# Performance work log

Measured on AMD Instinct MI355X. Metric: run time of the kernel, lower is better.

## Reference

```python
import jax, jax.numpy as jnp
import numpy as np

B, H, W, N, C = 2, 56, 56, 2, 128
NUM_HEADS = 8
SPLIT = 7
IDX = 0  # 0 -> H_sp = H, W_sp = split_size (vertical stripes)


def setup_inputs() -> dict:
    key = jax.random.key(0)
    k1, k2, k3, k4 = jax.random.split(key, 4)
    query = jax.random.normal(k1, (B, H, W, N, C), jnp.float32)
    key_t = jax.random.normal(k2, (B, H, W, N, C), jnp.float32)
    value = jax.random.normal(k3, (B, H, W, N, C), jnp.float32)
    conv_w = jax.random.normal(k4, (C, 1, 3, 3), jnp.float32) * 0.1  # depthwise get_v weight
    return {"query": query, "key": key_t, "value": value, "conv_w": conv_w}


def _im2cswin(x, Hsp, Wsp, h):
    # [b, Hp, Wp, n, c] -> [(b i j), h, Hsp*Wsp*n, d]
    b, Hp, Wp, n, c = x.shape
    i, j = Hp // Hsp, Wp // Wsp
    d = c // h
    x = x.reshape(b, i, Hsp, j, Wsp, n, h, d)
    x = x.transpose(0, 1, 3, 6, 2, 4, 5, 7)  # b i j h Hsp Wsp n d
    return x.reshape(b * i * j, h, Hsp * Wsp * n, d)


def _window_mask(Hsp, Wsp, n):
    # block attention between same spatial position / different candidates (except diagonal)
    pos = jnp.repeat(jnp.arange(Hsp * Wsp), n)
    L = pos.shape[0]
    m = jnp.where(pos[:, None] == pos[None, :], -jnp.inf, 0.0).astype(jnp.float32)
    m = m.at[jnp.arange(L), jnp.arange(L)].set(0.0)
    return m


def reference(query, key, value, conv_w):
    b, Hh, Ww, n, c = query.shape
    if IDX == -1:
        Hsp, Wsp = Hh, Ww
    elif IDX == 0:
        Hsp, Wsp = Hh, SPLIT
    else:
        Hsp, Wsp = SPLIT, Ww
    # H % Hsp == 0 and W % Wsp == 0 by construction -> no padding branch
    h = NUM_HEADS
    d = c // h
    scale = d ** (-0.5)

    q = _im2cswin(query, Hsp, Wsp, h)
    k = _im2cswin(key, Hsp, Wsp, h)
    v = _im2cswin(value, Hsp, Wsp, h)

    # rpe via depthwise 3x3 conv over the value (LePE-style), summed over candidates
    v_img = value.transpose(0, 3, 4, 1, 2).reshape(b * n, c, Hh, Ww)  # [b*n, C, H, W]
    conv = jax.lax.conv_general_dilated(
        v_img, conv_w, (1, 1), 'SAME',
        dimension_numbers=('NCHW', 'OIHW', 'NCHW'), feature_group_count=c)
    rpe = conv.reshape(b, n, c, Hh, Ww).sum(1, keepdims=True)
    center = conv_w[:, 0, 1, 1]  # center tap of each depthwise kernel
    self_scaled = (v_img * center[None, :, None, None]).reshape(b, n, c, Hh, Ww)
    self_scaled = self_scaled - self_scaled.sum(1, keepdims=True)
    rpe = (rpe + self_scaled).transpose(0, 3, 4, 1, 2)  # [b, H, W, n, c]

    mask = _window_mask(Hsp, Wsp, n)[None, None]  # [1,1,L,L]
    attn = jnp.einsum('bhid,bhjd->bhij', q * scale, k) + mask
    attn = jax.nn.softmax(attn.astype(jnp.float32), axis=-1).astype(q.dtype)
    x = jnp.einsum('bhij,bhjd->bhid', attn, v)

    # windows back to image layout
    i, j = Hh // Hsp, Ww // Wsp
    x = x.reshape(b, i, j, h, Hsp, Wsp, n, d)
    x = x.transpose(0, 1, 4, 2, 5, 6, 3, 7).reshape(b, Hh, Ww, n, c)
    return x + rpe
```

## Files before the change

kernel.cpp:

```cpp
#include <hip/hip_runtime.h>

typedef __bf16 bf16x8 __attribute__((ext_vector_type(8)));
typedef float f32x16 __attribute__((ext_vector_type(16)));
typedef unsigned u32x2 __attribute__((ext_vector_type(2)));

#define BB 2
#define HH 56
#define WW 56
#define NN 2
#define CC 128
#define NH 8
#define DD 16
#define WSP 7
#define LQ 784
#define KB_TOK 800
#define VT_STRIDE 808
#define NKC 25
#define NINST 128
#define BPI 5
#define NWAVE 5

#define K_OFF 0
#define V_OFF 25600
#define W_OFF 51456
#define ONES_OFF 52032
#define SMEM_BYTES 52064

#define QSCALE 0.3606737602222409f

union U2 { __bf16 h[2]; unsigned u; };
union U4 { unsigned u[4]; bf16x8 v; };
union H8 { bf16x8 v; uint4 q; };

static __device__ __forceinline__ float4 f4zero() { float4 r; r.x = r.y = r.z = r.w = 0.f; return r; }
static __device__ __forceinline__ float4 f4add(float4 a, float4 b) {
    float4 r; r.x = a.x + b.x; r.y = a.y + b.y; r.z = a.z + b.z; r.w = a.w + b.w; return r;
}
static __device__ __forceinline__ float4 f4fma(float4 acc, float4 w, float4 s) {
    acc.x += w.x * s.x; acc.y += w.y * s.y; acc.z += w.z * s.z; acc.w += w.w * s.w; return acc;
}

__global__ __launch_bounds__(320) void attn_fused(const float* __restrict__ q_g,
                                                  const float* __restrict__ k_g,
                                                  const float* __restrict__ v_g,
                                                  const float* __restrict__ conv_w,
                                                  float* __restrict__ out) {
    __shared__ alignas(16) char smem[SMEM_BYTES];
    __bf16* Klds = (__bf16*)(smem + K_OFF);
    __bf16* Vlds = (__bf16*)(smem + V_OFF);
    float*  wlds = (float*)(smem + W_OFF);
    __bf16* onesb = (__bf16*)(smem + ONES_OFF);

    const int bid  = blockIdx.x;
    const int g    = bid >> 3;
    const int inst = (bid & 7) + 8 * (g / BPI);
    const int part = g % BPI;
    const int head = inst & 7;
    const int win  = inst >> 3;
    const int b    = win >> 3, wj = win & 7;
    const int tid  = threadIdx.x;

    if (tid < 144) {
        int c = tid & 15, k = tid >> 4;
        wlds[k * 16 + c] = conv_w[(head * 16 + c) * 9 + k];
    } else if (tid < 160) {
        onesb[tid - 144] = (__bf16)1.f;
    }

    for (int tok = tid; tok < KB_TOK; tok += 320) {
        if (tok < LQ) {
            int pos = tok >> 1, n = tok & 1;
            int y = pos / WSP, xl2 = pos - y * WSP;
            long off = ((long)(((b * HH + y) * WW + wj * WSP + xl2) * NN + n)) * CC + head * DD;

            float kv[16], vv[16];
            *(float4*)&kv[0]  = *(const float4*)(k_g + off);
            *(float4*)&kv[4]  = *(const float4*)(k_g + off + 4);
            *(float4*)&kv[8]  = *(const float4*)(k_g + off + 8);
            *(float4*)&kv[12] = *(const float4*)(k_g + off + 12);
            *(float4*)&vv[0]  = *(const float4*)(v_g + off);
            *(float4*)&vv[4]  = *(const float4*)(v_g + off + 4);
            *(float4*)&vv[8]  = *(const float4*)(v_g + off + 8);
            *(float4*)&vv[12] = *(const float4*)(v_g + off + 12);

            H8 lo, hi;
#pragma unroll
            for (int i = 0; i < 8; ++i) { lo.v[i] = (__bf16)kv[i]; hi.v[i] = (__bf16)kv[8 + i]; }
            *(uint4*)&Klds[tok * 16]     = lo.q;
            *(uint4*)&Klds[tok * 16 + 8] = hi.q;
#pragma unroll
            for (int d = 0; d < 16; ++d)
                Vlds[d * VT_STRIDE + tok] = (__bf16)vv[d];
        } else {
            H8 z; z.q = make_uint4(0, 0, 0, 0);
            *(uint4*)&Klds[tok * 16]     = z.q;
            *(uint4*)&Klds[tok * 16 + 8] = z.q;
#pragma unroll
            for (int d = 0; d < 16; ++d)
                Vlds[d * VT_STRIDE + tok] = (__bf16)0.f;
        }
    }
    __syncthreads();

    const int w    = tid >> 6;
    const int lane = tid & 63;
    const int col  = lane & 31;
    const int h    = lane >> 5;
    const int qt   = part * NWAVE + w;
    const int myq  = qt * 32 + col;
    const int sib  = myq ^ 1;

    const int myqc = myq < LQ ? myq : LQ - 1;
    const int pos = myqc >> 1, n = myqc & 1;
    const int y = pos / WSP, xl = pos - y * WSP;
    const long ooff = ((long)(((b * HH + y) * WW + wj * WSP + xl) * NN + n)) * CC + head * DD;

    bf16x8 qfv;
    {
        const float* qp = q_g + ooff + 8 * h;
        float qv[8];
        *(float4*)&qv[0] = *(const float4*)qp;
        *(float4*)&qv[4] = *(const float4*)(qp + 4);
        H8 qq;
#pragma unroll
        for (int i = 0; i < 8; ++i) qq.v[i] = (__bf16)(qv[i] * QSCALE);
        qfv = qq.v;
    }

    f32x16 acc, zv;
#pragma unroll
    for (int i = 0; i < 16; ++i) { acc[i] = 0.f; zv[i] = 0.f; }

    const char* kbase = (const char*)Klds + col * 32 + h * 16;
    const char* vbase;
    int vstep, tstep;
    if (col < 16) {
        vbase = (const char*)Vlds + col * (VT_STRIDE * 2) + h * 16;
        vstep = 64; tstep = 32;
    } else {
        vbase = (const char*)onesb;
        vstep = 0; tstep = 0;
    }

    for (int c = 0; c < NKC; ++c) {
        bf16x8 kf = *(const bf16x8*)(kbase + c * 1024);

        f32x16 st = __builtin_amdgcn_mfma_f32_32x32x16_bf16(kf, qfv, zv, 0, 0, 0);

        float p[16];
        if (c == qt || c == NKC - 1) {
#pragma unroll
            for (int r = 0; r < 16; ++r) {
                int kr = (r & 3) + 8 * (r >> 2) + 4 * h;
                int gk = c * 32 + kr;
                p[r] = (gk >= LQ || gk == sib) ? 0.f : __builtin_amdgcn_exp2f(st[r]);
            }
        } else {
#pragma unroll
            for (int r = 0; r < 16; ++r) p[r] = __builtin_amdgcn_exp2f(st[r]);
        }

        unsigned pk[4][2];
#pragma unroll
        for (int b2 = 0; b2 < 4; ++b2) {
            U2 a, bb;
            a.h[0]  = (__bf16)p[4 * b2 + 0];
            a.h[1]  = (__bf16)p[4 * b2 + 1];
            bb.h[0] = (__bf16)p[4 * b2 + 2];
            bb.h[1] = (__bf16)p[4 * b2 + 3];
            pk[b2][0] = a.u;
            pk[b2][1] = bb.u;
        }

#pragma unroll
        for (int t = 0; t < 2; ++t) {
            U4 pb;
#pragma unroll
            for (int j = 0; j < 2; ++j) {
#if __has_builtin(__builtin_amdgcn_permlane32_swap)
                u32x2 rr = __builtin_amdgcn_permlane32_swap(pk[2 * t][j], pk[2 * t + 1][j], false, false);
                pb.u[j]     = rr[0];
                pb.u[2 + j] = rr[1];
#else
                unsigned swa = __shfl_xor(pk[2 * t][j], 32, 64);
                unsigned swb = __shfl_xor(pk[2 * t + 1][j], 32, 64);
                pb.u[j]     = h ? swb : pk[2 * t][j];
                pb.u[2 + j] = h ? pk[2 * t + 1][j] : swa;
#endif
            }
            bf16x8 vf = *(const bf16x8*)(vbase + c * vstep + t * tstep);
            acc = __builtin_amdgcn_mfma_f32_32x32x16_bf16(vf, pb.v, acc, 0, 0, 0);
        }
    }

    if (myq < LQ) {
        const int xg = wj * WSP + xl;
        const long rowbase = ((long)(b * HH + y) * WW + xg) * (NN * CC) + head * DD;

        float4 cv0 = f4zero(), cv1 = f4zero();
        float4 sc0 = f4zero(), sc1 = f4zero();
        float4 vn0 = f4zero(), vn1 = f4zero();

#pragma unroll
        for (int dy = -1; dy <= 1; ++dy) {
            int yy = y + dy;
#pragma unroll
            for (int dx = -1; dx <= 1; ++dx) {
                int xx = xg + dx;
                if (yy < 0 || yy >= HH || xx < 0 || xx >= WW) continue;
                int k = (dy + 1) * 3 + (dx + 1);
                const float* p = v_g + rowbase + ((long)dy * WW + dx) * (NN * CC);
                float4 a0 = *(const float4*)(p + 4 * h);
                float4 b0 = *(const float4*)(p + CC + 4 * h);
                float4 a1 = *(const float4*)(p + 8 + 4 * h);
                float4 b1 = *(const float4*)(p + CC + 8 + 4 * h);
                float4 w0 = *(const float4*)(wlds + k * 16 + 4 * h);
                float4 w1 = *(const float4*)(wlds + k * 16 + 8 + 4 * h);
                float4 S0 = f4add(a0, b0);
                float4 S1 = f4add(a1, b1);
                cv0 = f4fma(cv0, w0, S0);
                cv1 = f4fma(cv1, w1, S1);
                if (dy == 0 && dx == 0) {
                    sc0 = S0; sc1 = S1;
                    vn0 = n ? b0 : a0;
                    vn1 = n ? b1 : a1;
                }
            }
        }
        float4 wc0 = *(const float4*)(wlds + 4 * 16 + 4 * h);
        float4 wc1 = *(const float4*)(wlds + 4 * 16 + 8 + 4 * h);

        float inv = 1.f / acc[8];
        float* po = out + ooff;
        float4 r0, r1;
        r0.x = cv0.x + wc0.x * (vn0.x - sc0.x) + acc[0] * inv;
        r0.y = cv0.y + wc0.y * (vn0.y - sc0.y) + acc[1] * inv;
        r0.z = cv0.z + wc0.z * (vn0.z - sc0.z) + acc[2] * inv;
        r0.w = cv0.w + wc0.w * (vn0.w - sc0.w) + acc[3] * inv;
        r1.x = cv1.x + wc1.x * (vn1.x - sc1.x) + acc[4] * inv;
        r1.y = cv1.y + wc1.y * (vn1.y - sc1.y) + acc[5] * inv;
        r1.z = cv1.z + wc1.z * (vn1.z - sc1.z) + acc[6] * inv;
        r1.w = cv1.w + wc1.w * (vn1.w - sc1.w) + acc[7] * inv;
        *(float4*)(po + 4 * h) = r0;
        *(float4*)(po + 8 + 4 * h) = r1;
    }
}

extern "C" void kernel_launch(void* const* d_in, const int* in_sizes, int n_in,
                              void* d_out, int out_size, void* d_ws, size_t ws_size,
                              hipStream_t stream) {
    const float* q = (const float*)d_in[0];
    const float* k = (const float*)d_in[1];
    const float* v = (const float*)d_in[2];
    const float* w = (const float*)d_in[3];
    float* out = (float*)d_out;

    attn_fused<<<NINST * BPI, 320, 0, stream>>>(q, k, v, w, out);
}
```

Measured before the change: 37.71 us.

## Hoist depthwise conv before attention loop and split MFMA accumulator in two

Moves the LePE depthwise 3x3 conv gather from the epilogue to before the K/V staging loop. It uses branch-free clamped addresses with a zero multiplier, so its global loads overlap the LDS fill and the main loop instead of sitting serially at the end. The attention chunk loop is also unrolled into two independent accumulators, summed at the end, to break the MFMA accumulation dependency chain. In exchange, conv results stay live across the main loop, adding register pressure, and the loads at image borders are always issued.

```diff
diff --git a/kernel.cpp b/kernel.cpp
--- a/kernel.cpp
+++ b/kernel.cpp
@@ -36,8 +36,8 @@
 static __device__ __forceinline__ float4 f4add(float4 a, float4 b) {
     float4 r; r.x = a.x + b.x; r.y = a.y + b.y; r.z = a.z + b.z; r.w = a.w + b.w; return r;
 }
-static __device__ __forceinline__ float4 f4fma(float4 acc, float4 w, float4 s) {
-    acc.x += w.x * s.x; acc.y += w.y * s.y; acc.z += w.z * s.z; acc.w += w.w * s.w; return acc;
+static __device__ __forceinline__ float4 f4fmas(float4 acc, float4 w, float s, float4 S) {
+    acc.x += w.x * s * S.x; acc.y += w.y * s * S.y; acc.z += w.z * s * S.z; acc.w += w.w * s * S.w; return acc;
 }
 
 __global__ __launch_bounds__(320) void attn_fused(const float* __restrict__ q_g,
@@ -66,12 +66,57 @@
     } else if (tid < 160) {
         onesb[tid - 144] = (__bf16)1.f;
     }
+    __syncthreads();
+
+    const int w    = tid >> 6;
+    const int lane = tid & 63;
+    const int col  = lane & 31;
+    const int h    = lane >> 5;
+    const int qt   = part * NWAVE + w;
+    const int myq  = qt * 32 + col;
+    const int sib  = myq ^ 1;
+
+    const int myqc = myq < LQ ? myq : LQ - 1;
+    const int pos = myqc >> 1, n = myqc & 1;
+    const int y = pos / WSP, xl = pos - y * WSP;
+    const long ooff = ((long)(((b * HH + y) * WW + wj * WSP + xl) * NN + n)) * CC + head * DD;
+
+    float4 cv0 = f4zero(), cv1 = f4zero();
+    float4 sc0, sc1, vn0, vn1;
+    {
+        const int xg = wj * WSP + xl;
+        const long rowbase = ((long)(b * HH + y) * WW + xg) * (NN * CC) + head * DD;
+#pragma unroll
+        for (int k = 0; k < 9; ++k) {
+            int dy = k / 3 - 1, dx = k % 3 - 1;
+            int yy = y + dy, xx = xg + dx;
+            bool ok = (yy >= 0 && yy < HH && xx >= 0 && xx < WW);
+            int yc = ok ? yy : y, xc = ok ? xx : xg;
+            float m = ok ? 1.f : 0.f;
+            const float* p = v_g + rowbase + ((long)(yc - y) * WW + (xc - xg)) * (NN * CC);
+            float4 a0 = *(const float4*)(p + 4 * h);
+            float4 b0 = *(const float4*)(p + CC + 4 * h);
+            float4 a1 = *(const float4*)(p + 8 + 4 * h);
+            float4 b1 = *(const float4*)(p + CC + 8 + 4 * h);
+            float4 w0 = *(const float4*)(wlds + k * 16 + 4 * h);
+            float4 w1 = *(const float4*)(wlds + k * 16 + 8 + 4 * h);
+            float4 S0 = f4add(a0, b0);
+            float4 S1 = f4add(a1, b1);
+            cv0 = f4fmas(cv0, w0, m, S0);
+            cv1 = f4fmas(cv1, w1, m, S1);
+            if (k == 4) {
+                sc0 = S0; sc1 = S1;
+                vn0 = n ? b0 : a0;
+                vn1 = n ? b1 : a1;
+            }
+        }
+    }
 
     for (int tok = tid; tok < KB_TOK; tok += 320) {
         if (tok < LQ) {
-            int pos = tok >> 1, n = tok & 1;
-            int y = pos / WSP, xl2 = pos - y * WSP;
-            long off = ((long)(((b * HH + y) * WW + wj * WSP + xl2) * NN + n)) * CC + head * DD;
+            int tpos = tok >> 1, tn = tok & 1;
+            int ty = tpos / WSP, txl = tpos - ty * WSP;
+            long off = ((long)(((b * HH + ty) * WW + wj * WSP + txl) * NN + tn)) * CC + head * DD;
 
             float kv[16], vv[16];
             *(float4*)&kv[0]  = *(const float4*)(k_g + off);
@@ -102,19 +147,6 @@
     }
     __syncthreads();
 
-    const int w    = tid >> 6;
-    const int lane = tid & 63;
-    const int col  = lane & 31;
-    const int h    = lane >> 5;
-    const int qt   = part * NWAVE + w;
-    const int myq  = qt * 32 + col;
-    const int sib  = myq ^ 1;
-
-    const int myqc = myq < LQ ? myq : LQ - 1;
-    const int pos = myqc >> 1, n = myqc & 1;
-    const int y = pos / WSP, xl = pos - y * WSP;
-    const long ooff = ((long)(((b * HH + y) * WW + wj * WSP + xl) * NN + n)) * CC + head * DD;
-
     bf16x8 qfv;
     {
         const float* qp = q_g + ooff + 8 * h;
@@ -127,9 +159,9 @@
         qfv = qq.v;
     }
 
-    f32x16 acc, zv;
-#pragma unroll
-    for (int i = 0; i < 16; ++i) { acc[i] = 0.f; zv[i] = 0.f; }
+    f32x16 acc0, acc1, zv;
+#pragma unroll
+    for (int i = 0; i < 16; ++i) { acc0[i] = 0.f; acc1[i] = 0.f; zv[i] = 0.f; }
 
     const char* kbase = (const char*)Klds + col * 32 + h * 16;
     const char* vbase;
@@ -142,9 +174,8 @@
         vstep = 0; tstep = 0;
     }
 
-    for (int c = 0; c < NKC; ++c) {
+    auto do_chunk = [&](int c, f32x16& acc) {
         bf16x8 kf = *(const bf16x8*)(kbase + c * 1024);
-
         f32x16 st = __builtin_amdgcn_mfma_f32_32x32x16_bf16(kf, qfv, zv, 0, 0, 0);
 
         float p[16];
@@ -191,56 +222,29 @@
             bf16x8 vf = *(const bf16x8*)(vbase + c * vstep + t * tstep);
             acc = __builtin_amdgcn_mfma_f32_32x32x16_bf16(vf, pb.v, acc, 0, 0, 0);
         }
-    }
+    };
+
+    for (int it = 0; it < 12; ++it) {
+        do_chunk(2 * it, acc0);
+        do_chunk(2 * it + 1, acc1);
+    }
+    do_chunk(24, acc0);
 
     if (myq < LQ) {
-        const int xg = wj * WSP + xl;
-        const long rowbase = ((long)(b * HH + y) * WW + xg) * (NN * CC) + head * DD;
-
-        float4 cv0 = f4zero(), cv1 = f4zero();
-        float4 sc0 = f4zero(), sc1 = f4zero();
-        float4 vn0 = f4zero(), vn1 = f4zero();
-
-#pragma unroll
-        for (int dy = -1; dy <= 1; ++dy) {
-            int yy = y + dy;
-#pragma unroll
-            for (int dx = -1; dx <= 1; ++dx) {
-                int xx = xg + dx;
-                if (yy < 0 || yy >= HH || xx < 0 || xx >= WW) continue;
-                int k = (dy + 1) * 3 + (dx + 1);
-                const float* p = v_g + rowbase + ((long)dy * WW + dx) * (NN * CC);
-                float4 a0 = *(const float4*)(p + 4 * h);
-                float4 b0 = *(const float4*)(p + CC + 4 * h);
-                float4 a1 = *(const float4*)(p + 8 + 4 * h);
-                float4 b1 = *(const float4*)(p + CC + 8 + 4 * h);
-                float4 w0 = *(const float4*)(wlds + k * 16 + 4 * h);
-                float4 w1 = *(const float4*)(wlds + k * 16 + 8 + 4 * h);
-                float4 S0 = f4add(a0, b0);
-                float4 S1 = f4add(a1, b1);
-                cv0 = f4fma(cv0, w0, S0);
-                cv1 = f4fma(cv1, w1, S1);
-                if (dy == 0 && dx == 0) {
-                    sc0 = S0; sc1 = S1;
-                    vn0 = n ? b0 : a0;
-                    vn1 = n ? b1 : a1;
-                }
-            }
-        }
+        float lsum = acc0[8] + acc1[8];
+        float inv = 1.f / lsum;
         float4 wc0 = *(const float4*)(wlds + 4 * 16 + 4 * h);
         float4 wc1 = *(const float4*)(wlds + 4 * 16 + 8 + 4 * h);
-
-        float inv = 1.f / acc[8];
         float* po = out + ooff;
         float4 r0, r1;
-        r0.x = cv0.x + wc0.x * (vn0.x - sc0.x) + acc[0] * inv;
-        r0.y = cv0.y + wc0.y * (vn0.y - sc0.y) + acc[1] * inv;
-        r0.z = cv0.z + wc0.z * (vn0.z - sc0.z) + acc[2] * inv;
-        r0.w = cv0.w + wc0.w * (vn0.w - sc0.w) + acc[3] * inv;
-        r1.x = cv1.x + wc1.x * (vn1.x - sc1.x) + acc[4] * inv;
-        r1.y = cv1.y + wc1.y * (vn1.y - sc1.y) + acc[5] * inv;
-        r1.z = cv1.z + wc1.z * (vn1.z - sc1.z) + acc[6] * inv;
-        r1.w = cv1.w + wc1.w * (vn1.w - sc1.w) + acc[7] * inv;
+        r0.x = cv0.x + wc0.x * (vn0.x - sc0.x) + (acc0[0] + acc1[0]) * inv;
+        r0.y = cv0.y + wc0.y * (vn0.y - sc0.y) + (acc0[1] + acc1[1]) * inv;
+        r0.z = cv0.z + wc0.z * (vn0.z - sc0.z) + (acc0[2] + acc1[2]) * inv;
+        r0.w = cv0.w + wc0.w * (vn0.w - sc0.w) + (acc0[3] + acc1[3]) * inv;
+        r1.x = cv1.x + wc1.x * (vn1.x - sc1.x) + (acc0[4] + acc1[4]) * inv;
+        r1.y = cv1.y + wc1.y * (vn1.y - sc1.y) + (acc0[5] + acc1[5]) * inv;
+        r1.z = cv1.z + wc1.z * (vn1.z - sc1.z) + (acc0[6] + acc1[6]) * inv;
+        r1.w = cv1.w + wc1.w * (vn1.w - sc1.w) + (acc0[7] + acc1[7]) * inv;
         *(float4*)(po + 4 * h) = r0;
         *(float4*)(po + 8 + 4 * h) = r1;
     }
```

Measured after the change: 61.28 us. +62.5%, slower.

## Split key loop across two waves per query tile and load K directly from global

Applied to the files above, without the earlier changes.

Doubles the block to 640 threads so each 32-query tile is handled by two waves that process alternating key chunks, then combines their partial accumulators through shared memory before the epilogue. K is no longer staged in LDS; each wave loads and converts its key fragment straight from global memory inside the loop, which shrinks LDS usage. The intent is more parallelism and shorter per-wave serial loops. In exchange it adds an extra barrier and reduction step, and puts scattered global K loads on the critical path of the MFMA loop.

```diff
diff --git a/kernel.cpp b/kernel.cpp
--- a/kernel.cpp
+++ b/kernel.cpp
@@ -18,13 +18,13 @@
 #define NKC 25
 #define NINST 128
 #define BPI 5
-#define NWAVE 5
-
-#define K_OFF 0
-#define V_OFF 25600
-#define W_OFF 51456
-#define ONES_OFF 52032
-#define SMEM_BYTES 52064
+#define NTHR 640
+
+#define V_OFF 0
+#define W_OFF 25856
+#define ONES_OFF 26432
+#define RED_OFF 26464
+#define SMEM_BYTES 39264
 
 #define QSCALE 0.3606737602222409f
 
@@ -40,16 +40,16 @@
     acc.x += w.x * s.x; acc.y += w.y * s.y; acc.z += w.z * s.z; acc.w += w.w * s.w; return acc;
 }
 
-__global__ __launch_bounds__(320) void attn_fused(const float* __restrict__ q_g,
-                                                  const float* __restrict__ k_g,
-                                                  const float* __restrict__ v_g,
-                                                  const float* __restrict__ conv_w,
-                                                  float* __restrict__ out) {
+__global__ __launch_bounds__(NTHR) void attn_fused(const float* __restrict__ q_g,
+                                                   const float* __restrict__ k_g,
+                                                   const float* __restrict__ v_g,
+                                                   const float* __restrict__ conv_w,
+                                                   float* __restrict__ out) {
     __shared__ alignas(16) char smem[SMEM_BYTES];
-    __bf16* Klds = (__bf16*)(smem + K_OFF);
-    __bf16* Vlds = (__bf16*)(smem + V_OFF);
-    float*  wlds = (float*)(smem + W_OFF);
+    __bf16* Vlds  = (__bf16*)(smem + V_OFF);
+    float*  wlds  = (float*)(smem + W_OFF);
     __bf16* onesb = (__bf16*)(smem + ONES_OFF);
+    float*  red   = (float*)(smem + RED_OFF);
 
     const int bid  = blockIdx.x;
     const int g    = bid >> 3;
@@ -67,34 +67,20 @@
         onesb[tid - 144] = (__bf16)1.f;
     }
 
-    for (int tok = tid; tok < KB_TOK; tok += 320) {
+    for (int tok = tid; tok < KB_TOK; tok += NTHR) {
         if (tok < LQ) {
-            int pos = tok >> 1, n = tok & 1;
-            int y = pos / WSP, xl2 = pos - y * WSP;
-            long off = ((long)(((b * HH + y) * WW + wj * WSP + xl2) * NN + n)) * CC + head * DD;
-
-            float kv[16], vv[16];
-            *(float4*)&kv[0]  = *(const float4*)(k_g + off);
-            *(float4*)&kv[4]  = *(const float4*)(k_g + off + 4);
-            *(float4*)&kv[8]  = *(const float4*)(k_g + off + 8);
-            *(float4*)&kv[12] = *(const float4*)(k_g + off + 12);
+            int tpos = tok >> 1, tn = tok & 1;
+            int ty = tpos / WSP, txl = tpos - ty * WSP;
+            long off = ((long)(((b * HH + ty) * WW + wj * WSP + txl) * NN + tn)) * CC + head * DD;
+            float vv[16];
             *(float4*)&vv[0]  = *(const float4*)(v_g + off);
             *(float4*)&vv[4]  = *(const float4*)(v_g + off + 4);
             *(float4*)&vv[8]  = *(const float4*)(v_g + off + 8);
             *(float4*)&vv[12] = *(const float4*)(v_g + off + 12);
-
-            H8 lo, hi;
-#pragma unroll
-            for (int i = 0; i < 8; ++i) { lo.v[i] = (__bf16)kv[i]; hi.v[i] = (__bf16)kv[8 + i]; }
-            *(uint4*)&Klds[tok * 16]     = lo.q;
-            *(uint4*)&Klds[tok * 16 + 8] = hi.q;
 #pragma unroll
             for (int d = 0; d < 16; ++d)
                 Vlds[d * VT_STRIDE + tok] = (__bf16)vv[d];
         } else {
-            H8 z; z.q = make_uint4(0, 0, 0, 0);
-            *(uint4*)&Klds[tok * 16]     = z.q;
-            *(uint4*)&Klds[tok * 16 + 8] = z.q;
 #pragma unroll
             for (int d = 0; d < 16; ++d)
                 Vlds[d * VT_STRIDE + tok] = (__bf16)0.f;
@@ -102,13 +88,15 @@
     }
     __syncthreads();
 
-    const int w    = tid >> 6;
-    const int lane = tid & 63;
-    const int col  = lane & 31;
-    const int h    = lane >> 5;
-    const int qt   = part * NWAVE + w;
-    const int myq  = qt * 32 + col;
-    const int sib  = myq ^ 1;
+    const int w     = tid >> 6;
+    const int lane  = tid & 63;
+    const int col   = lane & 31;
+    const int h     = lane >> 5;
+    const int tile  = w >> 1;
+    const int khalf = w & 1;
+    const int qt    = part * BPI + tile;
+    const int myq   = qt * 32 + col;
+    const int sib   = myq ^ 1;
 
     const int myqc = myq < LQ ? myq : LQ - 1;
     const int pos = myqc >> 1, n = myqc & 1;
@@ -131,7 +119,6 @@
 #pragma unroll
     for (int i = 0; i < 16; ++i) { acc[i] = 0.f; zv[i] = 0.f; }
 
-    const char* kbase = (const char*)Klds + col * 32 + h * 16;
     const char* vbase;
     int vstep, tstep;
     if (col < 16) {
@@ -142,8 +129,22 @@
         vstep = 0; tstep = 0;
     }
 
-    for (int c = 0; c < NKC; ++c) {
-        bf16x8 kf = *(const bf16x8*)(kbase + c * 1024);
+    for (int c = khalf; c < NKC; c += 2) {
+        bf16x8 kf;
+        {
+            int tok = c * 32 + col;
+            int tokc = tok < LQ ? tok : LQ - 1;
+            int tpos = tokc >> 1, tn = tokc & 1;
+            int ty = tpos / WSP, txl = tpos - ty * WSP;
+            long koff = ((long)(((b * HH + ty) * WW + wj * WSP + txl) * NN + tn)) * CC + head * DD + 8 * h;
+            float kv[8];
+            *(float4*)&kv[0] = *(const float4*)(k_g + koff);
+            *(float4*)&kv[4] = *(const float4*)(k_g + koff + 4);
+            H8 kk;
+#pragma unroll
+            for (int i = 0; i < 8; ++i) kk.v[i] = (__bf16)kv[i];
+            kf = kk.v;
+        }
 
         f32x16 st = __builtin_amdgcn_mfma_f32_32x32x16_bf16(kf, qfv, zv, 0, 0, 0);
 
@@ -193,7 +194,20 @@
         }
     }
 
-    if (myq < LQ) {
+    if (khalf) {
+        float* rp = red + (tile * 64 + lane) * 10;
+#pragma unroll
+        for (int i = 0; i < 9; ++i) rp[i] = acc[i];
+    }
+    __syncthreads();
+
+    if (!khalf && myq < LQ) {
+        const float* rp = red + (tile * 64 + lane) * 10;
+        float o[9];
+#pragma unroll
+        for (int i = 0; i < 9; ++i) o[i] = acc[i] + rp[i];
+        float inv = 1.f / o[8];
+
         const int xg = wj * WSP + xl;
         const long rowbase = ((long)(b * HH + y) * WW + xg) * (NN * CC) + head * DD;
 
@@ -230,17 +244,16 @@
         float4 wc0 = *(const float4*)(wlds + 4 * 16 + 4 * h);
         float4 wc1 = *(const float4*)(wlds + 4 * 16 + 8 + 4 * h);
 
-        float inv = 1.f / acc[8];
         float* po = out + ooff;
         float4 r0, r1;
-        r0.x = cv0.x + wc0.x * (vn0.x - sc0.x) + acc[0] * inv;
-        r0.y = cv0.y + wc0.y * (vn0.y - sc0.y) + acc[1] * inv;
-        r0.z = cv0.z + wc0.z * (vn0.z - sc0.z) + acc[2] * inv;
-        r0.w = cv0.w + wc0.w * (vn0.w - sc0.w) + acc[3] * inv;
-        r1.x = cv1.x + wc1.x * (vn1.x - sc1.x) + acc[4] * inv;
-        r1.y = cv1.y + wc1.y * (vn1.y - sc1.y) + acc[5] * inv;
-        r1.z = cv1.z + wc1.z * (vn1.z - sc1.z) + acc[6] * inv;
-        r1.w = cv1.w + wc1.w * (vn1.w - sc1.w) + acc[7] * inv;
+        r0.x = cv0.x + wc0.x * (vn0.x - sc0.x) + o[0] * inv;
+        r0.y = cv0.y + wc0.y * (vn0.y - sc0.y) + o[1] * inv;
+        r0.z = cv0.z + wc0.z * (vn0.z - sc0.z) + o[2] * inv;
+        r0.w = cv0.w + wc0.w * (vn0.w - sc0.w) + o[3] * inv;
+        r1.x = cv1.x + wc1.x * (vn1.x - sc1.x) + o[4] * inv;
+        r1.y = cv1.y + wc1.y * (vn1.y - sc1.y) + o[5] * inv;
+        r1.z = cv1.z + wc1.z * (vn1.z - sc1.z) + o[6] * inv;
+        r1.w = cv1.w + wc1.w * (vn1.w - sc1.w) + o[7] * inv;
         *(float4*)(po + 4 * h) = r0;
         *(float4*)(po + 8 + 4 * h) = r1;
     }
@@ -255,5 +268,5 @@
     const float* w = (const float*)d_in[3];
     float* out = (float*)d_out;
 
-    attn_fused<<<NINST * BPI, 320, 0, stream>>>(q, k, v, w, out);
-}
+    attn_fused<<<NINST * BPI, NTHR, 0, stream>>>(q, k, v, w, out);
+}
```

Measured after the change: 45.51 us. 1.21x slower.

## Pre-pack K to bf16 in workspace and read K fragments directly from global

Applied to the files above, without the earlier changes.

Adds a separate pack_k kernel that converts K to bf16 in per-window/head token order in the workspace. The attention kernel no longer stages K in LDS; each wave reads its MFMA K fragments straight from the packed global buffer, which halves LDS use and may allow more resident blocks. The cost is an extra launch plus a global round-trip for K. The fragment loads now sit inside the main loop and rely on cache hits, since five blocks share each instance's K.

```diff
diff --git a/kernel.cpp b/kernel.cpp
--- a/kernel.cpp
+++ b/kernel.cpp
@@ -19,12 +19,12 @@
 #define NINST 128
 #define BPI 5
 #define NWAVE 5
-
-#define K_OFF 0
-#define V_OFF 25600
-#define W_OFF 51456
-#define ONES_OFF 52032
-#define SMEM_BYTES 52064
+#define KW_UNITS 1600
+
+#define V_OFF 0
+#define W_OFF 25856
+#define ONES_OFF 26432
+#define SMEM_BYTES 26464
 
 #define QSCALE 0.3606737602222409f
 
@@ -40,15 +40,45 @@
     acc.x += w.x * s.x; acc.y += w.y * s.y; acc.z += w.z * s.z; acc.w += w.w * s.w; return acc;
 }
 
+__global__ __launch_bounds__(256) void pack_k(const float* __restrict__ k_g,
+                                              uint4* __restrict__ kws) {
+    int idx = blockIdx.x * blockDim.x + threadIdx.x;
+    if (idx >= NINST * KB_TOK) return;
+    int inst = idx / KB_TOK;
+    int tok  = idx - inst * KB_TOK;
+    uint4* dst = kws + (long)inst * KW_UNITS + tok * 2;
+
+    if (tok >= LQ) {
+        uint4 z = make_uint4(0, 0, 0, 0);
+        dst[0] = z; dst[1] = z;
+        return;
+    }
+    int head = inst & 7, win = inst >> 3;
+    int b = win >> 3, wj = win & 7;
+    int pos = tok >> 1, n = tok & 1;
+    int y = pos / WSP, xl = pos - y * WSP;
+    long off = ((long)(((b * HH + y) * WW + wj * WSP + xl) * NN + n)) * CC + head * DD;
+
+    float kv[16];
+    *(float4*)&kv[0]  = *(const float4*)(k_g + off);
+    *(float4*)&kv[4]  = *(const float4*)(k_g + off + 4);
+    *(float4*)&kv[8]  = *(const float4*)(k_g + off + 8);
+    *(float4*)&kv[12] = *(const float4*)(k_g + off + 12);
+    H8 lo, hi;
+#pragma unroll
+    for (int i = 0; i < 8; ++i) { lo.v[i] = (__bf16)kv[i]; hi.v[i] = (__bf16)kv[8 + i]; }
+    dst[0] = lo.q;
+    dst[1] = hi.q;
+}
+
 __global__ __launch_bounds__(320) void attn_fused(const float* __restrict__ q_g,
-                                                  const float* __restrict__ k_g,
+                                                  const uint4* __restrict__ kws,
                                                   const float* __restrict__ v_g,
                                                   const float* __restrict__ conv_w,
                                                   float* __restrict__ out) {
     __shared__ alignas(16) char smem[SMEM_BYTES];
-    __bf16* Klds = (__bf16*)(smem + K_OFF);
-    __bf16* Vlds = (__bf16*)(smem + V_OFF);
-    float*  wlds = (float*)(smem + W_OFF);
+    __bf16* Vlds  = (__bf16*)(smem + V_OFF);
+    float*  wlds  = (float*)(smem + W_OFF);
     __bf16* onesb = (__bf16*)(smem + ONES_OFF);
 
     const int bid  = blockIdx.x;
@@ -69,32 +99,18 @@
 
     for (int tok = tid; tok < KB_TOK; tok += 320) {
         if (tok < LQ) {
-            int pos = tok >> 1, n = tok & 1;
-            int y = pos / WSP, xl2 = pos - y * WSP;
-            long off = ((long)(((b * HH + y) * WW + wj * WSP + xl2) * NN + n)) * CC + head * DD;
-
-            float kv[16], vv[16];
-            *(float4*)&kv[0]  = *(const float4*)(k_g + off);
-            *(float4*)&kv[4]  = *(const float4*)(k_g + off + 4);
-            *(float4*)&kv[8]  = *(const float4*)(k_g + off + 8);
-            *(float4*)&kv[12] = *(const float4*)(k_g + off + 12);
+            int tpos = tok >> 1, tn = tok & 1;
+            int ty = tpos / WSP, txl = tpos - ty * WSP;
+            long off = ((long)(((b * HH + ty) * WW + wj * WSP + txl) * NN + tn)) * CC + head * DD;
+            float vv[16];
             *(float4*)&vv[0]  = *(const float4*)(v_g + off);
             *(float4*)&vv[4]  = *(const float4*)(v_g + off + 4);
             *(float4*)&vv[8]  = *(const float4*)(v_g + off + 8);
             *(float4*)&vv[12] = *(const float4*)(v_g + off + 12);
-
-            H8 lo, hi;
-#pragma unroll
-            for (int i = 0; i < 8; ++i) { lo.v[i] = (__bf16)kv[i]; hi.v[i] = (__bf16)kv[8 + i]; }
-            *(uint4*)&Klds[tok * 16]     = lo.q;
-            *(uint4*)&Klds[tok * 16 + 8] = hi.q;
 #pragma unroll
             for (int d = 0; d < 16; ++d)
                 Vlds[d * VT_STRIDE + tok] = (__bf16)vv[d];
         } else {
-            H8 z; z.q = make_uint4(0, 0, 0, 0);
-            *(uint4*)&Klds[tok * 16]     = z.q;
-            *(uint4*)&Klds[tok * 16 + 8] = z.q;
 #pragma unroll
             for (int d = 0; d < 16; ++d)
                 Vlds[d * VT_STRIDE + tok] = (__bf16)0.f;
@@ -131,7 +147,7 @@
 #pragma unroll
     for (int i = 0; i < 16; ++i) { acc[i] = 0.f; zv[i] = 0.f; }
 
-    const char* kbase = (const char*)Klds + col * 32 + h * 16;
+    const uint4* kbase = kws + (long)inst * KW_UNITS + (col * 2 + h);
     const char* vbase;
     int vstep, tstep;
     if (col < 16) {
@@ -143,9 +159,9 @@
     }
 
     for (int c = 0; c < NKC; ++c) {
-        bf16x8 kf = *(const bf16x8*)(kbase + c * 1024);
-
-        f32x16 st = __builtin_amdgcn_mfma_f32_32x32x16_bf16(kf, qfv, zv, 0, 0, 0);
+        U4 kf;
+        *(uint4*)&kf = kbase[c * 64];
+        f32x16 st = __builtin_amdgcn_mfma_f32_32x32x16_bf16(kf.v, qfv, zv, 0, 0, 0);
 
         float p[16];
         if (c == qt || c == NKC - 1) {
@@ -194,6 +210,8 @@
     }
 
     if (myq < LQ) {
+        float inv = 1.f / acc[8];
+
         const int xg = wj * WSP + xl;
         const long rowbase = ((long)(b * HH + y) * WW + xg) * (NN * CC) + head * DD;
 
@@ -230,7 +248,6 @@
         float4 wc0 = *(const float4*)(wlds + 4 * 16 + 4 * h);
         float4 wc1 = *(const float4*)(wlds + 4 * 16 + 8 + 4 * h);
 
-        float inv = 1.f / acc[8];
         float* po = out + ooff;
         float4 r0, r1;
         r0.x = cv0.x + wc0.x * (vn0.x - sc0.x) + acc[0] * inv;
@@ -254,6 +271,10 @@
     const float* v = (const float*)d_in[2];
     const float* w = (const float*)d_in[3];
     float* out = (float*)d_out;
-
-    attn_fused<<<NINST * BPI, 320, 0, stream>>>(q, k, v, w, out);
-}
+    uint4* kws = (uint4*)d_ws;
+
+    int n1 = NINST * KB_TOK;
+    pack_k<<<(n1 + 255) / 256, 256, 0, stream>>>(k, kws);
+
+    attn_fused<<<NINST * BPI, 320, 0, stream>>>(q, kws, v, w, out);
+}
```

New measurement: 39.97 us. +6.0%, slower.
